# Kernel optimization log

Hardware: AMD Instinct MI355X
Metric: run time of the kernel (lower is better)

The kernel has to match this reference:

```python
import jax, jax.numpy as jnp
import numpy as np

B, N, IN, OUT = 16, 1000, 128, 128


def setup_inputs() -> dict:
    key = jax.random.key(0)
    ks = jax.random.split(key, 8)
    stdv = 1.0 / np.sqrt(IN + OUT)  # matches reset_param uniform(-stdv, stdv)
    def w(k):
        return jax.random.uniform(k, (N, IN + OUT, OUT), jnp.float32, -stdv, stdv)
    return {
        "xt": jax.random.normal(ks[0], (B, N, IN), jnp.float32),
        "hidden": jax.random.normal(ks[1], (1, N, OUT), jnp.float32),
        "ct_1": jax.random.normal(ks[2], (1, N, OUT), jnp.float32),
        "W_i": w(ks[3]), "b_i": jnp.zeros((N, OUT), jnp.float32),
        "W_o": w(ks[4]), "b_o": jnp.zeros((N, OUT), jnp.float32),
        "W_f": w(ks[5]), "b_f": jnp.zeros((N, OUT), jnp.float32),
        "W_c": w(ks[6]), "b_c": jnp.zeros((N, OUT), jnp.float32),
    }


def reference(xt, hidden, ct_1, W_i, b_i, W_o, b_o, W_f, b_f, W_c, b_c):
    b = xt.shape[0]
    h = jnp.broadcast_to(hidden, (b,) + hidden.shape[1:])       # [B,N,OUT]
    xh = jnp.concatenate([xt, h], axis=-1)                      # [B,N,IN+OUT]

    def gate(W, bias, act):
        # per-stock batched matmul: [B,N,K] x [N,K,O] -> [B,N,O]
        return act(jnp.einsum('bnk,nko->bno', xh, W) + bias)

    it = gate(W_i, b_i, jax.nn.sigmoid)
    ot = gate(W_o, b_o, jax.nn.sigmoid)
    ft = gate(W_f, b_f, jax.nn.sigmoid)
    chat = gate(W_c, b_c, jnp.tanh)

    ct = ft * jnp.broadcast_to(ct_1, it.shape) + it * chat
    ht = ot * jnp.tanh(ct)
    return ht, ct
```

## Files before the change

### kernel.cpp

```cpp
#include <hip/hip_runtime.h>
#include <hip/hip_bf16.h>

namespace {
constexpr int B   = 16;
constexpr int NS  = 1000;
constexpr int IN  = 128;
constexpr int OUT = 128;
constexpr int K   = 256;

__device__ __forceinline__ float fsigmoid(float x) {
  return 1.0f / (1.0f + __expf(-x));
}
__device__ __forceinline__ float ftanh(float x) {
  return 2.0f / (1.0f + __expf(-2.0f * x)) - 1.0f;
}

__global__ __launch_bounds__(256, 4) void lstm_kernel(
    const float* __restrict__ xt, const float* __restrict__ hidden,
    const float* __restrict__ ct_1,
    const float* __restrict__ Wi, const float* __restrict__ bi,
    const float* __restrict__ Wo, const float* __restrict__ bo,
    const float* __restrict__ Wf, const float* __restrict__ bfp,
    const float* __restrict__ Wc, const float* __restrict__ bc,
    float* __restrict__ out) {
  __shared__ float smem[4 * B * OUT];
  float (*xh)[K] = (float (*)[K])smem;

  const int n = blockIdx.x;
  const int tid = threadIdx.x;

  #pragma unroll
  for (int r = 0; r < 2; ++r) {
    const int idx = tid + (r << 8);
    const int b = idx >> 5;
    const int j = (idx & 31) << 2;
    const float4 xv = *reinterpret_cast<const float4*>(
        xt + ((size_t)b * NS + n) * IN + j);
    *reinterpret_cast<float4*>(&xh[b][j]) = xv;
    const float4 hv = *reinterpret_cast<const float4*>(
        hidden + (size_t)n * OUT + j);
    *reinterpret_cast<float4*>(&xh[b][IN + j]) = hv;
  }
  __syncthreads();

  const int g  = tid >> 6;
  const int ol = tid & 63;

  const float* Wg = (g == 0) ? Wi : (g == 1) ? Wo : (g == 2) ? Wf : Wc;
  const float* bg = (g == 0) ? bi : (g == 1) ? bo : (g == 2) ? bfp : bc;
  const float* wp = Wg + (size_t)n * (K * OUT) + ol;

  float acc0[B], acc1[B];
  #pragma unroll
  for (int b = 0; b < B; ++b) { acc0[b] = 0.f; acc1[b] = 0.f; }

  #pragma unroll 2
  for (int k = 0; k < K; k += 4) {
    float w0[4], w1[4];
    #pragma unroll
    for (int q = 0; q < 4; ++q) {
      w0[q] = wp[(size_t)(k + q) * OUT];
      w1[q] = wp[(size_t)(k + q) * OUT + 64];
    }
    #pragma unroll
    for (int b = 0; b < B; ++b) {
      const float4 x = *reinterpret_cast<const float4*>(&xh[b][k]);
      acc0[b] = fmaf(x.x, w0[0], acc0[b]);
      acc0[b] = fmaf(x.y, w0[1], acc0[b]);
      acc0[b] = fmaf(x.z, w0[2], acc0[b]);
      acc0[b] = fmaf(x.w, w0[3], acc0[b]);
      acc1[b] = fmaf(x.x, w1[0], acc1[b]);
      acc1[b] = fmaf(x.y, w1[1], acc1[b]);
      acc1[b] = fmaf(x.z, w1[2], acc1[b]);
      acc1[b] = fmaf(x.w, w1[3], acc1[b]);
    }
  }

  const float bias0 = bg[(size_t)n * OUT + ol];
  const float bias1 = bg[(size_t)n * OUT + ol + 64];

  __syncthreads();
  #pragma unroll
  for (int b = 0; b < B; ++b) {
    smem[((g * B + b) << 7) + ol]      = acc0[b] + bias0;
    smem[((g * B + b) << 7) + ol + 64] = acc1[b] + bias1;
  }
  __syncthreads();

  const size_t nbase = (size_t)n * OUT;
  #pragma unroll
  for (int r = 0; r < 8; ++r) {
    const int p = tid + (r << 8);
    const int b = p >> 7;
    const int o = p & 127;
    const float gi = smem[((0 * B + b) << 7) + o];
    const float go = smem[((1 * B + b) << 7) + o];
    const float gf = smem[((2 * B + b) << 7) + o];
    const float gc = smem[((3 * B + b) << 7) + o];
    const float it = fsigmoid(gi);
    const float ot = fsigmoid(go);
    const float ft = fsigmoid(gf);
    const float ch = ftanh(gc);
    const float cp = ct_1[nbase + o];
    const float ct = ft * cp + it * ch;
    const float ht = ot * ftanh(ct);
    const size_t oidx = (size_t)b * ((size_t)NS * OUT) + nbase + o;
    out[oidx] = ht;
    out[(size_t)B * NS * OUT + oidx] = ct;
  }
}
}

extern "C" void kernel_launch(void* const* d_in, const int* in_sizes, int n_in,
                              void* d_out, int out_size, void* d_ws, size_t ws_size,
                              hipStream_t stream) {
  const float* xt     = (const float*)d_in[0];
  const float* hidden = (const float*)d_in[1];
  const float* ct_1   = (const float*)d_in[2];
  const float* Wi     = (const float*)d_in[3];
  const float* bi     = (const float*)d_in[4];
  const float* Wo     = (const float*)d_in[5];
  const float* bo     = (const float*)d_in[6];
  const float* Wf     = (const float*)d_in[7];
  const float* bf     = (const float*)d_in[8];
  const float* Wc     = (const float*)d_in[9];
  const float* bc     = (const float*)d_in[10];

  lstm_kernel<<<NS, 256, 0, stream>>>(xt, hidden, ct_1, Wi, bi, Wo, bo,
                                      Wf, bf, Wc, bc,
                                      (float*)d_out);
}
```

Before: 112.9 us.

## Retile per-gate matmul as 4x8 register tiles with vectorized weight loads

Each thread now computes a 4-batch by 8-output register tile instead of 16 batches by 2 outputs, loading weights as float4 pairs instead of scalar strided loads. The xh rows are padded to 260 floats to reduce LDS bank conflicts, since threads in a wavefront now read different batch rows. The aim is fewer, wider global weight loads. The cost is that weights are now read redundantly by the four batch-quarter groups, though L1/L2 should absorb this.

```diff
diff --git a/kernel.cpp b/kernel.cpp
--- a/kernel.cpp
+++ b/kernel.cpp
@@ -7,6 +7,7 @@
 constexpr int IN  = 128;
 constexpr int OUT = 128;
 constexpr int K   = 256;
+constexpr int XHP = 260;
 
 __device__ __forceinline__ float fsigmoid(float x) {
   return 1.0f / (1.0f + __expf(-x));
@@ -24,7 +25,6 @@
     const float* __restrict__ Wc, const float* __restrict__ bc,
     float* __restrict__ out) {
   __shared__ float smem[4 * B * OUT];
-  float (*xh)[K] = (float (*)[K])smem;
 
   const int n = blockIdx.x;
   const int tid = threadIdx.x;
@@ -36,54 +36,68 @@
     const int j = (idx & 31) << 2;
     const float4 xv = *reinterpret_cast<const float4*>(
         xt + ((size_t)b * NS + n) * IN + j);
-    *reinterpret_cast<float4*>(&xh[b][j]) = xv;
+    *reinterpret_cast<float4*>(&smem[b * XHP + j]) = xv;
     const float4 hv = *reinterpret_cast<const float4*>(
         hidden + (size_t)n * OUT + j);
-    *reinterpret_cast<float4*>(&xh[b][IN + j]) = hv;
+    *reinterpret_cast<float4*>(&smem[b * XHP + IN + j]) = hv;
   }
   __syncthreads();
 
   const int g  = tid >> 6;
-  const int ol = tid & 63;
+  const int q  = (tid >> 4) & 3;
+  const int cl = tid & 15;
 
   const float* Wg = (g == 0) ? Wi : (g == 1) ? Wo : (g == 2) ? Wf : Wc;
   const float* bg = (g == 0) ? bi : (g == 1) ? bo : (g == 2) ? bfp : bc;
-  const float* wp = Wg + (size_t)n * (K * OUT) + ol;
+  const float* wp = Wg + (size_t)n * (K * OUT) + cl * 8;
 
-  float acc0[B], acc1[B];
+  float acc[4][8];
   #pragma unroll
-  for (int b = 0; b < B; ++b) { acc0[b] = 0.f; acc1[b] = 0.f; }
+  for (int bi2 = 0; bi2 < 4; ++bi2)
+    #pragma unroll
+    for (int ci = 0; ci < 8; ++ci) acc[bi2][ci] = 0.f;
 
   #pragma unroll 2
   for (int k = 0; k < K; k += 4) {
-    float w0[4], w1[4];
+    float4 w[4][2];
     #pragma unroll
-    for (int q = 0; q < 4; ++q) {
-      w0[q] = wp[(size_t)(k + q) * OUT];
-      w1[q] = wp[(size_t)(k + q) * OUT + 64];
+    for (int kk = 0; kk < 4; ++kk) {
+      w[kk][0] = *reinterpret_cast<const float4*>(wp + (size_t)(k + kk) * OUT);
+      w[kk][1] = *reinterpret_cast<const float4*>(wp + (size_t)(k + kk) * OUT + 4);
     }
     #pragma unroll
-    for (int b = 0; b < B; ++b) {
-      const float4 x = *reinterpret_cast<const float4*>(&xh[b][k]);
-      acc0[b] = fmaf(x.x, w0[0], acc0[b]);
-      acc0[b] = fmaf(x.y, w0[1], acc0[b]);
-      acc0[b] = fmaf(x.z, w0[2], acc0[b]);
-      acc0[b] = fmaf(x.w, w0[3], acc0[b]);
-      acc1[b] = fmaf(x.x, w1[0], acc1[b]);
-      acc1[b] = fmaf(x.y, w1[1], acc1[b]);
-      acc1[b] = fmaf(x.z, w1[2], acc1[b]);
-      acc1[b] = fmaf(x.w, w1[3], acc1[b]);
+    for (int bi2 = 0; bi2 < 4; ++bi2) {
+      const float4 x = *reinterpret_cast<const float4*>(
+          &smem[(q * 4 + bi2) * XHP + k]);
+      #pragma unroll
+      for (int ci = 0; ci < 4; ++ci) {
+        acc[bi2][ci]     = fmaf(x.x, (&w[0][0].x)[ci], acc[bi2][ci]);
+        acc[bi2][ci]     = fmaf(x.y, (&w[1][0].x)[ci], acc[bi2][ci]);
+        acc[bi2][ci]     = fmaf(x.z, (&w[2][0].x)[ci], acc[bi2][ci]);
+        acc[bi2][ci]     = fmaf(x.w, (&w[3][0].x)[ci], acc[bi2][ci]);
+        acc[bi2][ci + 4] = fmaf(x.x, (&w[0][1].x)[ci], acc[bi2][ci + 4]);
+        acc[bi2][ci + 4] = fmaf(x.y, (&w[1][1].x)[ci], acc[bi2][ci + 4]);
+        acc[bi2][ci + 4] = fmaf(x.z, (&w[2][1].x)[ci], acc[bi2][ci + 4]);
+        acc[bi2][ci + 4] = fmaf(x.w, (&w[3][1].x)[ci], acc[bi2][ci + 4]);
+      }
     }
   }
 
-  const float bias0 = bg[(size_t)n * OUT + ol];
-  const float bias1 = bg[(size_t)n * OUT + ol + 64];
+  float bias[8];
+  #pragma unroll
+  for (int ci = 0; ci < 8; ++ci) bias[ci] = bg[(size_t)n * OUT + cl * 8 + ci];
 
   __syncthreads();
   #pragma unroll
-  for (int b = 0; b < B; ++b) {
-    smem[((g * B + b) << 7) + ol]      = acc0[b] + bias0;
-    smem[((g * B + b) << 7) + ol + 64] = acc1[b] + bias1;
+  for (int bi2 = 0; bi2 < 4; ++bi2) {
+    const int b = q * 4 + bi2;
+    float4 v0, v1;
+    v0.x = acc[bi2][0] + bias[0]; v0.y = acc[bi2][1] + bias[1];
+    v0.z = acc[bi2][2] + bias[2]; v0.w = acc[bi2][3] + bias[3];
+    v1.x = acc[bi2][4] + bias[4]; v1.y = acc[bi2][5] + bias[5];
+    v1.z = acc[bi2][6] + bias[6]; v1.w = acc[bi2][7] + bias[7];
+    *reinterpret_cast<float4*>(&smem[((g * B + b) << 7) + cl * 8])     = v0;
+    *reinterpret_cast<float4*>(&smem[((g * B + b) << 7) + cl * 8 + 4]) = v1;
   }
   __syncthreads();
 
```

Result: slower. 131.3 us (+16.3%).

## Split K across half-waves with float4 weight loads and register prefetch

Applied to the files above, without the earlier changes.

Each thread now computes four adjacent output columns with float4 weight loads, and the two half-waves each take half of every 8-wide K chunk. The partial sums are combined with a cross-lane shuffle. Weights for the next chunk are prefetched into registers, and the xh rows in shared memory are padded to a stride of 260 floats. This aims to cut the number of global load instructions and hide load latency, at the cost of a shuffle reduction and more register pressure.

```diff
diff --git a/kernel.cpp b/kernel.cpp
--- a/kernel.cpp
+++ b/kernel.cpp
@@ -7,6 +7,7 @@
 constexpr int IN  = 128;
 constexpr int OUT = 128;
 constexpr int K   = 256;
+constexpr int XHP = 260;
 
 __device__ __forceinline__ float fsigmoid(float x) {
   return 1.0f / (1.0f + __expf(-x));
@@ -24,7 +25,6 @@
     const float* __restrict__ Wc, const float* __restrict__ bc,
     float* __restrict__ out) {
   __shared__ float smem[4 * B * OUT];
-  float (*xh)[K] = (float (*)[K])smem;
 
   const int n = blockIdx.x;
   const int tid = threadIdx.x;
@@ -36,54 +36,74 @@
     const int j = (idx & 31) << 2;
     const float4 xv = *reinterpret_cast<const float4*>(
         xt + ((size_t)b * NS + n) * IN + j);
-    *reinterpret_cast<float4*>(&xh[b][j]) = xv;
+    *reinterpret_cast<float4*>(&smem[b * XHP + j]) = xv;
     const float4 hv = *reinterpret_cast<const float4*>(
         hidden + (size_t)n * OUT + j);
-    *reinterpret_cast<float4*>(&xh[b][IN + j]) = hv;
+    *reinterpret_cast<float4*>(&smem[b * XHP + IN + j]) = hv;
   }
   __syncthreads();
 
-  const int g  = tid >> 6;
-  const int ol = tid & 63;
+  const int g    = tid >> 6;
+  const int lane = tid & 63;
+  const int kc   = lane >> 5;
+  const int cg   = lane & 31;
 
   const float* Wg = (g == 0) ? Wi : (g == 1) ? Wo : (g == 2) ? Wf : Wc;
   const float* bg = (g == 0) ? bi : (g == 1) ? bo : (g == 2) ? bfp : bc;
-  const float* wp = Wg + (size_t)n * (K * OUT) + ol;
+  const float* wp = Wg + (size_t)n * (K * OUT) + cg * 4;
 
-  float acc0[B], acc1[B];
+  float acc[B][4];
   #pragma unroll
-  for (int b = 0; b < B; ++b) { acc0[b] = 0.f; acc1[b] = 0.f; }
+  for (int b = 0; b < B; ++b)
+    #pragma unroll
+    for (int c = 0; c < 4; ++c) acc[b][c] = 0.f;
+
+  float4 wv[4];
+  #pragma unroll
+  for (int j = 0; j < 4; ++j)
+    wv[j] = *reinterpret_cast<const float4*>(wp + (size_t)(kc * 4 + j) * OUT);
 
   #pragma unroll 2
-  for (int k = 0; k < K; k += 4) {
-    float w0[4], w1[4];
+  for (int k = 0; k < K; k += 8) {
+    const int kn = (k + 8 < K) ? (k + 8) : 0;
+    float4 nv[4];
     #pragma unroll
-    for (int q = 0; q < 4; ++q) {
-      w0[q] = wp[(size_t)(k + q) * OUT];
-      w1[q] = wp[(size_t)(k + q) * OUT + 64];
+    for (int j = 0; j < 4; ++j)
+      nv[j] = *reinterpret_cast<const float4*>(wp + (size_t)(kn + kc * 4 + j) * OUT);
+
+    #pragma unroll
+    for (int b = 0; b < B; ++b) {
+      const float4 xv = *reinterpret_cast<const float4*>(&smem[b * XHP + k + kc * 4]);
+      #pragma unroll
+      for (int j = 0; j < 4; ++j) {
+        const float xs = (&xv.x)[j];
+        acc[b][0] = fmaf(xs, wv[j].x, acc[b][0]);
+        acc[b][1] = fmaf(xs, wv[j].y, acc[b][1]);
+        acc[b][2] = fmaf(xs, wv[j].z, acc[b][2]);
+        acc[b][3] = fmaf(xs, wv[j].w, acc[b][3]);
+      }
     }
     #pragma unroll
-    for (int b = 0; b < B; ++b) {
-      const float4 x = *reinterpret_cast<const float4*>(&xh[b][k]);
-      acc0[b] = fmaf(x.x, w0[0], acc0[b]);
-      acc0[b] = fmaf(x.y, w0[1], acc0[b]);
-      acc0[b] = fmaf(x.z, w0[2], acc0[b]);
-      acc0[b] = fmaf(x.w, w0[3], acc0[b]);
-      acc1[b] = fmaf(x.x, w1[0], acc1[b]);
-      acc1[b] = fmaf(x.y, w1[1], acc1[b]);
-      acc1[b] = fmaf(x.z, w1[2], acc1[b]);
-      acc1[b] = fmaf(x.w, w1[3], acc1[b]);
-    }
+    for (int j = 0; j < 4; ++j) wv[j] = nv[j];
   }
 
-  const float bias0 = bg[(size_t)n * OUT + ol];
-  const float bias1 = bg[(size_t)n * OUT + ol + 64];
+  #pragma unroll
+  for (int b = 0; b < B; ++b)
+    #pragma unroll
+    for (int c = 0; c < 4; ++c)
+      acc[b][c] += __shfl_xor(acc[b][c], 32, 64);
+
+  const float4 bv = *reinterpret_cast<const float4*>(bg + (size_t)n * OUT + cg * 4);
 
   __syncthreads();
-  #pragma unroll
-  for (int b = 0; b < B; ++b) {
-    smem[((g * B + b) << 7) + ol]      = acc0[b] + bias0;
-    smem[((g * B + b) << 7) + ol + 64] = acc1[b] + bias1;
+  if (kc == 0) {
+    #pragma unroll
+    for (int b = 0; b < B; ++b) {
+      float4 v;
+      v.x = acc[b][0] + bv.x; v.y = acc[b][1] + bv.y;
+      v.z = acc[b][2] + bv.z; v.w = acc[b][3] + bv.w;
+      *reinterpret_cast<float4*>(&smem[((g * B + b) << 7) + cg * 4]) = v;
+    }
   }
   __syncthreads();
 
```

Measured after the change: 123.7 us. +9.5%, slower.

## Compute per-stock gate matmuls with bf16 MFMA instead of fp32 FMAs

Applied to the files above, without the earlier changes.

Converts the xh activations and the fp32 weights to bf16 in LDS, using swizzled layouts, and computes each gate's 16x128x256 product with mfma_f32_16x16x32_bf16. The block grows to 512 threads, with two waves per gate each covering 64 output columns. The aim is to shift the inner product from the vector FMA units onto the matrix cores. In exchange, weights must be converted to bf16 on every call, which costs extra ALU and LDS traffic, and rounding inputs to bf16 lowers accuracy. The kernel is likely still limited by weight bandwidth, since about 131 MB of fp32 weights are read per call.

```diff
diff --git a/kernel.cpp b/kernel.cpp
--- a/kernel.cpp
+++ b/kernel.cpp
@@ -8,14 +8,25 @@
 constexpr int OUT = 128;
 constexpr int K   = 256;
 
+typedef __attribute__((ext_vector_type(8))) short short8;
+typedef __attribute__((ext_vector_type(4))) float f32x4;
+
 __device__ __forceinline__ float fsigmoid(float x) {
   return 1.0f / (1.0f + __expf(-x));
 }
 __device__ __forceinline__ float ftanh(float x) {
   return 2.0f / (1.0f + __expf(-2.0f * x)) - 1.0f;
 }
+__device__ __forceinline__ unsigned int f2bf(float f) {
+  unsigned int u = __builtin_bit_cast(unsigned int, f);
+  u += 0x7fffu + ((u >> 16) & 1u);
+  return u >> 16;
+}
+__device__ __forceinline__ unsigned int pack2(float lo, float hi) {
+  return f2bf(lo) | (f2bf(hi) << 16);
+}
 
-__global__ __launch_bounds__(256, 4) void lstm_kernel(
+__global__ __launch_bounds__(512, 2) void lstm_kernel(
     const float* __restrict__ xt, const float* __restrict__ hidden,
     const float* __restrict__ ct_1,
     const float* __restrict__ Wi, const float* __restrict__ bi,
@@ -23,80 +34,98 @@
     const float* __restrict__ Wf, const float* __restrict__ bfp,
     const float* __restrict__ Wc, const float* __restrict__ bc,
     float* __restrict__ out) {
-  __shared__ float smem[4 * B * OUT];
-  float (*xh)[K] = (float (*)[K])smem;
+  __shared__ __align__(16) unsigned char smem[40960];
 
-  const int n = blockIdx.x;
+  const int n   = blockIdx.x;
   const int tid = threadIdx.x;
 
-  #pragma unroll
-  for (int r = 0; r < 2; ++r) {
-    const int idx = tid + (r << 8);
-    const int b = idx >> 5;
-    const int j = (idx & 31) << 2;
-    const float4 xv = *reinterpret_cast<const float4*>(
-        xt + ((size_t)b * NS + n) * IN + j);
-    *reinterpret_cast<float4*>(&xh[b][j]) = xv;
-    const float4 hv = *reinterpret_cast<const float4*>(
-        hidden + (size_t)n * OUT + j);
-    *reinterpret_cast<float4*>(&xh[b][IN + j]) = hv;
+  {
+    const int b  = tid >> 5;
+    const int s  = tid & 31;
+    const int k0 = s << 3;
+    float v[8];
+    if (k0 < IN) {
+      const float4 a = *reinterpret_cast<const float4*>(xt + ((size_t)b * NS + n) * IN + k0);
+      const float4 c = *reinterpret_cast<const float4*>(xt + ((size_t)b * NS + n) * IN + k0 + 4);
+      v[0]=a.x; v[1]=a.y; v[2]=a.z; v[3]=a.w; v[4]=c.x; v[5]=c.y; v[6]=c.z; v[7]=c.w;
+    } else {
+      const float4 a = *reinterpret_cast<const float4*>(hidden + (size_t)n * OUT + (k0 - IN));
+      const float4 c = *reinterpret_cast<const float4*>(hidden + (size_t)n * OUT + (k0 - IN) + 4);
+      v[0]=a.x; v[1]=a.y; v[2]=a.z; v[3]=a.w; v[4]=c.x; v[5]=c.y; v[6]=c.z; v[7]=c.w;
+    }
+    uint4 pk;
+    pk.x = pack2(v[0], v[1]); pk.y = pack2(v[2], v[3]);
+    pk.z = pack2(v[4], v[5]); pk.w = pack2(v[6], v[7]);
+    const int addr = ((b << 9) + (s << 4)) ^ ((b & 7) << 4);
+    *reinterpret_cast<uint4*>(&smem[addr]) = pk;
   }
   __syncthreads();
 
-  const int g  = tid >> 6;
-  const int ol = tid & 63;
+  const int wid  = tid >> 6;
+  const int g    = wid >> 1;
+  const int half = wid & 1;
+  const int l    = tid & 63;
+  const int g2   = l >> 4;
+  const int c16  = l & 15;
 
   const float* Wg = (g == 0) ? Wi : (g == 1) ? Wo : (g == 2) ? Wf : Wc;
   const float* bg = (g == 0) ? bi : (g == 1) ? bo : (g == 2) ? bfp : bc;
-  const float* wp = Wg + (size_t)n * (K * OUT) + ol;
+  const float* wgp = Wg + (size_t)n * (K * OUT) + half * 64 + l;
 
-  float acc0[B], acc1[B];
+  const int wsl = 8192 + (wid << 12);
+  f32x4 acc[4] = {f32x4{0,0,0,0}, f32x4{0,0,0,0}, f32x4{0,0,0,0}, f32x4{0,0,0,0}};
+
   #pragma unroll
-  for (int b = 0; b < B; ++b) { acc0[b] = 0.f; acc1[b] = 0.f; }
-
-  #pragma unroll 2
-  for (int k = 0; k < K; k += 4) {
-    float w0[4], w1[4];
+  for (int c = 0; c < 8; ++c) {
+    float wr[8][4];
     #pragma unroll
-    for (int q = 0; q < 4; ++q) {
-      w0[q] = wp[(size_t)(k + q) * OUT];
-      w1[q] = wp[(size_t)(k + q) * OUT + 64];
+    for (int i = 0; i < 8; ++i)
+      #pragma unroll
+      for (int j = 0; j < 4; ++j)
+        wr[i][j] = wgp[(size_t)((c << 5) + (i << 2) + j) * OUT];
+    #pragma unroll
+    for (int i = 0; i < 8; ++i) {
+      uint2 pw;
+      pw.x = pack2(wr[i][0], wr[i][1]);
+      pw.y = pack2(wr[i][2], wr[i][3]);
+      const int a = (wsl + (l << 6) + (i << 3)) ^ ((l & 7) << 4);
+      *reinterpret_cast<uint2*>(&smem[a]) = pw;
     }
+    const int aaddr = ((c16 << 9) + (c << 6) + (g2 << 4)) ^ ((c16 & 7) << 4);
+    const short8 af = *reinterpret_cast<const short8*>(&smem[aaddr]);
     #pragma unroll
-    for (int b = 0; b < B; ++b) {
-      const float4 x = *reinterpret_cast<const float4*>(&xh[b][k]);
-      acc0[b] = fmaf(x.x, w0[0], acc0[b]);
-      acc0[b] = fmaf(x.y, w0[1], acc0[b]);
-      acc0[b] = fmaf(x.z, w0[2], acc0[b]);
-      acc0[b] = fmaf(x.w, w0[3], acc0[b]);
-      acc1[b] = fmaf(x.x, w1[0], acc1[b]);
-      acc1[b] = fmaf(x.y, w1[1], acc1[b]);
-      acc1[b] = fmaf(x.z, w1[2], acc1[b]);
-      acc1[b] = fmaf(x.w, w1[3], acc1[b]);
+    for (int t = 0; t < 4; ++t) {
+      const int col   = (t << 4) + c16;
+      const int baddr = (wsl + (col << 6) + (g2 << 4)) ^ ((col & 7) << 4);
+      const short8 bf = *reinterpret_cast<const short8*>(&smem[baddr]);
+      acc[t] = __builtin_amdgcn_mfma_f32_16x16x32_bf16(af, bf, acc[t], 0, 0, 0);
     }
   }
 
-  const float bias0 = bg[(size_t)n * OUT + ol];
-  const float bias1 = bg[(size_t)n * OUT + ol + 64];
-
   __syncthreads();
+  float* gb = reinterpret_cast<float*>(&smem[8192]);
   #pragma unroll
-  for (int b = 0; b < B; ++b) {
-    smem[((g * B + b) << 7) + ol]      = acc0[b] + bias0;
-    smem[((g * B + b) << 7) + ol + 64] = acc1[b] + bias1;
+  for (int t = 0; t < 4; ++t) {
+    const int colg = (half << 6) + (t << 4) + c16;
+    const float bias = bg[(size_t)n * OUT + colg];
+    #pragma unroll
+    for (int r = 0; r < 4; ++r) {
+      const int b = (g2 << 2) + r;
+      gb[g * 2048 + b * 128 + colg] = acc[t][r] + bias;
+    }
   }
   __syncthreads();
 
   const size_t nbase = (size_t)n * OUT;
   #pragma unroll
-  for (int r = 0; r < 8; ++r) {
-    const int p = tid + (r << 8);
+  for (int r = 0; r < 4; ++r) {
+    const int p = tid + (r << 9);
     const int b = p >> 7;
     const int o = p & 127;
-    const float gi = smem[((0 * B + b) << 7) + o];
-    const float go = smem[((1 * B + b) << 7) + o];
-    const float gf = smem[((2 * B + b) << 7) + o];
-    const float gc = smem[((3 * B + b) << 7) + o];
+    const float gi = gb[0 * 2048 + b * 128 + o];
+    const float go = gb[1 * 2048 + b * 128 + o];
+    const float gf = gb[2 * 2048 + b * 128 + o];
+    const float gc = gb[3 * 2048 + b * 128 + o];
     const float it = fsigmoid(gi);
     const float ot = fsigmoid(go);
     const float ft = fsigmoid(gf);
@@ -126,7 +155,7 @@
   const float* Wc     = (const float*)d_in[9];
   const float* bc     = (const float*)d_in[10];
 
-  lstm_kernel<<<NS, 256, 0, stream>>>(xt, hidden, ct_1, Wi, bi, Wo, bo,
+  lstm_kernel<<<NS, 512, 0, stream>>>(xt, hidden, ct_1, Wi, bi, Wo, bo,
                                       Wf, bf, Wc, bc,
                                       (float*)d_out);
 }
```

Measured after the change: 114.8 us. About the same (+1.6%).
